# Kernel optimization log

Measured on AMD Instinct MI355X. Metric: run time of the kernel, lower is better.

The kernel has to match this reference:

```python
import jax, jax.numpy as jnp
import numpy as np

N_NODES = 50000
N_EDGES = 400000
NUM_GRAPHS = 64
D = 128
NUM_ACTIONS = 40


def setup_inputs() -> dict:
    key = jax.random.key(0)
    ks = jax.random.split(key, 20)
    s = 1.0 / np.sqrt(D)
    inp = {
        'inputs': jax.random.normal(ks[0], (N_NODES, D), jnp.float32),
        'src': jax.random.randint(ks[1], (N_EDGES,), 0, N_NODES, jnp.int32),
        'dst': jax.random.randint(ks[2], (N_EDGES,), 0, N_NODES, jnp.int32),
        'graph_ids': jnp.sort(jax.random.randint(ks[3], (N_NODES,), 0, NUM_GRAPHS, jnp.int32)),
        'init_feats': jax.random.normal(ks[4], (N_NODES, D), jnp.float32),
        'init_graph_ids': jnp.sort(jax.random.randint(ks[5], (N_NODES,), 0, NUM_GRAPHS, jnp.int32)),
        'lead_feats': jax.random.normal(ks[6], (N_NODES, D), jnp.float32),
        'lead_graph_ids': jnp.sort(jax.random.randint(ks[7], (N_NODES,), 0, NUM_GRAPHS, jnp.int32)),
        'W1': jax.random.normal(ks[8], (D, D), jnp.float32) * s,
        'b1': jnp.zeros((D,), jnp.float32),
        'W2': jax.random.normal(ks[9], (D, D), jnp.float32) * s,
        'b2': jnp.zeros((D,), jnp.float32),
        'W3': jax.random.normal(ks[10], (D, D), jnp.float32) * s,
        'b3': jnp.zeros((D,), jnp.float32),
        'fc1_W': jax.random.normal(ks[11], (D, D), jnp.float32) * s,
        'fc1_b': jnp.zeros((D,), jnp.float32),
        'fc2_W': jax.random.normal(ks[12], (D, NUM_ACTIONS), jnp.float32) * s,
        'fc2_b': jnp.zeros((NUM_ACTIONS,), jnp.float32),
    }
    return inp


def _pool(feats, gids):
    # SumPooling over a batched graph -> [B, D]
    return jax.ops.segment_sum(feats, gids, num_segments=NUM_GRAPHS)


def _ggin_layer(h, src, dst, graph_ids, ctx_per_graph, W, b):
    # neighbor sum aggregation (message passing over edge list)
    agg = jax.ops.segment_sum(h[src], dst, num_segments=N_NODES)  # [N, D]
    h_global = _pool(h, graph_ids)                                # [B, D]
    ctx = (h_global + ctx_per_graph)[graph_ids]                   # broadcast per-graph context to nodes
    return (h + agg + ctx) @ W + b


def reference(inputs, src, dst, graph_ids, init_feats, init_graph_ids,
              lead_feats, lead_graph_ids, W1, b1, W2, b2, W3, b3,
              fc1_W, fc1_b, fc2_W, fc2_b):
    h_initial = _pool(init_feats, init_graph_ids)   # [B, D]
    h_lead = _pool(lead_feats, lead_graph_ids)      # [B, D]
    ctx = h_initial + h_lead

    h = jax.nn.relu(_ggin_layer(inputs, src, dst, graph_ids, ctx, W1, b1))
    h = jax.nn.relu(_ggin_layer(h, src, dst, graph_ids, ctx, W2, b2))
    h = jax.nn.relu(_ggin_layer(h, src, dst, graph_ids, ctx, W3, b3))

    h_global = _pool(h, graph_ids)                  # [B, D]
    h_fc = jax.nn.relu(h_global @ fc1_W + fc1_b)
    return h_fc @ fc2_W + fc2_b                     # [B, num_actions]
```

## Files before the change

kernel.cpp:

```cpp
#include <hip/hip_runtime.h>

#define D 128
#define NGRAPH 64
#define NACT 40
#define SCAN_TPB 256
#define SCAN_EPT 8
#define SCAN_CHUNK 2048
#define GNODES 8
#define POOL_CHUNK 64

typedef __attribute__((ext_vector_type(8))) short bf16x8;
typedef __attribute__((ext_vector_type(4))) float f32x4;
typedef __attribute__((ext_vector_type(8))) unsigned short us8;

__device__ inline unsigned short f2b(float f) {
    unsigned u = __float_as_uint(f);
    return (unsigned short)((u + 0x7FFFu + ((u >> 16) & 1u)) >> 16);
}
__device__ inline float b2f(unsigned short h) {
    return __uint_as_float(((unsigned)h) << 16);
}

__global__ void pool3_kernel(const float* __restrict__ f0, const int* __restrict__ g0, float* o0,
                             const float* __restrict__ f1, const int* __restrict__ g1, float* o1,
                             const float* __restrict__ f2, const int* __restrict__ g2, float* o2,
                             int n_nodes) {
    const float* feats; const int* gids; float* out;
    if (blockIdx.y == 0)      { feats = f0; gids = g0; out = o0; }
    else if (blockIdx.y == 1) { feats = f1; gids = g1; out = o1; }
    else                      { feats = f2; gids = g2; out = o2; }
    int t = threadIdx.x;
    int start = blockIdx.x * POOL_CHUNK;
    int end = start + POOL_CHUNK;
    if (end > n_nodes) end = n_nodes;
    if (start >= end) return;
    int cur = gids[start];
    float acc = 0.f;
    int r = start;
    while (r < end) {
        if (r + 3 < end && gids[r] == cur && gids[r + 3] == cur) {
            float v0 = feats[(size_t)r * D + t];
            float v1 = feats[(size_t)(r + 1) * D + t];
            float v2 = feats[(size_t)(r + 2) * D + t];
            float v3 = feats[(size_t)(r + 3) * D + t];
            acc += (v0 + v1) + (v2 + v3);
            r += 4;
            continue;
        }
        int g = gids[r];
        if (g != cur) { atomicAdd(&out[cur * D + t], acc); acc = 0.f; cur = g; }
        acc += feats[(size_t)r * D + t];
        ++r;
    }
    atomicAdd(&out[cur * D + t], acc);
}

__global__ void pool_b16_kernel(const unsigned short* __restrict__ feats,
                                const int* __restrict__ gids, float* __restrict__ out,
                                int n_nodes) {
    int t = threadIdx.x;
    int start = blockIdx.x * POOL_CHUNK;
    int end = start + POOL_CHUNK;
    if (end > n_nodes) end = n_nodes;
    if (start >= end) return;
    int cur = gids[start];
    float acc = 0.f;
    int r = start;
    while (r < end) {
        if (r + 3 < end && gids[r] == cur && gids[r + 3] == cur) {
            float v0 = b2f(feats[(size_t)r * D + t]);
            float v1 = b2f(feats[(size_t)(r + 1) * D + t]);
            float v2 = b2f(feats[(size_t)(r + 2) * D + t]);
            float v3 = b2f(feats[(size_t)(r + 3) * D + t]);
            acc += (v0 + v1) + (v2 + v3);
            r += 4;
            continue;
        }
        int g = gids[r];
        if (g != cur) { atomicAdd(&out[cur * D + t], acc); acc = 0.f; cur = g; }
        acc += b2f(feats[(size_t)r * D + t]);
        ++r;
    }
    atomicAdd(&out[cur * D + t], acc);
}

__global__ void ctxw_kernel(const float* __restrict__ hg, const float* __restrict__ ctx,
                            const float* __restrict__ W, const float* __restrict__ b,
                            float* __restrict__ out) {
    __shared__ float row[D];
    int g = blockIdx.x, t = threadIdx.x;
    row[t] = hg[g * D + t] + ctx[g * D + t];
    __syncthreads();
    float acc = b[t];
#pragma unroll 4
    for (int k = 0; k < D; ++k) acc = fmaf(row[k], W[k * D + t], acc);
    out[g * D + t] = acc;
}

__global__ void conv_kernel(const float4* __restrict__ in4, ushort4* __restrict__ out4, int n4) {
    int stride = gridDim.x * blockDim.x;
    for (int i = blockIdx.x * blockDim.x + threadIdx.x; i < n4; i += stride) {
        float4 v = in4[i];
        ushort4 o;
        o.x = f2b(v.x); o.y = f2b(v.y); o.z = f2b(v.z); o.w = f2b(v.w);
        out4[i] = o;
    }
}

__global__ void wconv_kernel(const float* __restrict__ W0, const float* __restrict__ W1,
                             const float* __restrict__ W2, unsigned short* __restrict__ WTb) {
    const float* W = blockIdx.y == 0 ? W0 : (blockIdx.y == 1 ? W1 : W2);
    unsigned short* WT = WTb + blockIdx.y * (D * D);
    int idx = blockIdx.x * 256 + threadIdx.x;
    int n = idx >> 7, k = idx & 127;
    WT[n * D + k] = f2b(W[k * D + n]);
}

__global__ __launch_bounds__(256) void mm_mfma(const unsigned short* __restrict__ Hb,
                                               const unsigned short* __restrict__ WT,
                                               unsigned short* __restrict__ X, int n_rows) {
    __shared__ unsigned short aT[64 * 136];
    __shared__ unsigned short bT[128 * 136];
    int t = threadIdx.x;
    int r0 = blockIdx.x * 64;

    for (int i = t; i < 1024; i += 256) {
        int r = i >> 4, kq = i & 15;
        us8 v = {0, 0, 0, 0, 0, 0, 0, 0};
        if (r0 + r < n_rows) v = *(const us8*)(Hb + (size_t)(r0 + r) * D + kq * 8);
        *(us8*)&aT[r * 136 + kq * 8] = v;
    }
    for (int i = t; i < 2048; i += 256) {
        int n = i >> 4, kq = i & 15;
        *(us8*)&bT[n * 136 + kq * 8] = *(const us8*)(WT + n * D + kq * 8);
    }
    __syncthreads();

    int lane = t & 63;
    int rbase = (t >> 6) * 16;
    int arow = lane & 15, kgrp = lane >> 4;
    f32x4 acc[8];
#pragma unroll
    for (int i = 0; i < 8; ++i) acc[i] = (f32x4){0.f, 0.f, 0.f, 0.f};

#pragma unroll
    for (int kc = 0; kc < 4; ++kc) {
        bf16x8 a = *(bf16x8*)&aT[(rbase + arow) * 136 + kc * 32 + kgrp * 8];
#pragma unroll
        for (int nt = 0; nt < 8; ++nt) {
            bf16x8 b = *(bf16x8*)&bT[(nt * 16 + arow) * 136 + kc * 32 + kgrp * 8];
            acc[nt] = __builtin_amdgcn_mfma_f32_16x16x32_bf16(a, b, acc[nt], 0, 0, 0);
        }
    }

    int rr = rbase + kgrp * 4;
#pragma unroll
    for (int nt = 0; nt < 8; ++nt) {
#pragma unroll
        for (int j = 0; j < 4; ++j) {
            int r = r0 + rr + j;
            if (r < n_rows) X[(size_t)r * D + nt * 16 + arow] = f2b(acc[nt][j]);
        }
    }
}

__global__ void hist_kernel(const int* __restrict__ dst, int* __restrict__ counts, int n_edges) {
    int stride = gridDim.x * blockDim.x;
    for (int e = blockIdx.x * blockDim.x + threadIdx.x; e < n_edges; e += stride)
        atomicAdd(&counts[dst[e]], 1);
}

__global__ void scanA_kernel(const int* __restrict__ counts, int* __restrict__ rowptr,
                             int* __restrict__ blocksums, int n) {
    __shared__ int smem[SCAN_TPB];
    int b = blockIdx.x, t = threadIdx.x;
    int i0 = b * SCAN_CHUNK + t * SCAN_EPT;
    int e[SCAN_EPT];
#pragma unroll
    for (int j = 0; j < SCAN_EPT; ++j) {
        int i = i0 + j;
        e[j] = (i < n) ? counts[i] : 0;
    }
#pragma unroll
    for (int j = 1; j < SCAN_EPT; ++j) e[j] += e[j - 1];
    smem[t] = e[SCAN_EPT - 1];
    __syncthreads();
    for (int off = 1; off < SCAN_TPB; off <<= 1) {
        int u = (t >= off) ? smem[t - off] : 0;
        __syncthreads();
        smem[t] += u;
        __syncthreads();
    }
    int excl = t ? smem[t - 1] : 0;
#pragma unroll
    for (int j = 0; j < SCAN_EPT; ++j) {
        int i = i0 + j;
        if (i < n) rowptr[i + 1] = excl + e[j];
    }
    if (t == SCAN_TPB - 1) blocksums[b] = smem[t];
    if (b == 0 && t == 0) rowptr[0] = 0;
}

__global__ void scanC_kernel(int* __restrict__ rowptr, int* __restrict__ cursor,
                             const int* __restrict__ blocksums, int n) {
    __shared__ int off_s;
    int b = blockIdx.x, t = threadIdx.x;
    if (t == 0) {
        int a = 0;
        for (int i = 0; i < b; ++i) a += blocksums[i];
        off_s = a;
    }
    __syncthreads();
    int off = off_s;
    int i0 = b * SCAN_CHUNK + t * SCAN_EPT;
#pragma unroll
    for (int j = 0; j < SCAN_EPT; ++j) {
        int i = i0 + j;
        if (i < n) {
            int v = rowptr[i + 1] + off;
            rowptr[i + 1] = v;
            if (i + 1 < n) cursor[i + 1] = v;
        }
    }
    if (b == 0 && t == 0) cursor[0] = 0;
}

__global__ void fill_kernel(const int* __restrict__ src, const int* __restrict__ dst,
                            int* __restrict__ cursor, int* __restrict__ srcs, int n_edges) {
    int stride = gridDim.x * blockDim.x;
    for (int e = blockIdx.x * blockDim.x + threadIdx.x; e < n_edges; e += stride) {
        int pos = atomicAdd(&cursor[dst[e]], 1);
        srcs[pos] = src[e];
    }
}

__global__ __launch_bounds__(256) void gather_kernel(const unsigned short* __restrict__ Xb,
        const int* __restrict__ rowptr, const int* __restrict__ srcs,
        const int* __restrict__ gids, const float4* __restrict__ ctxgW4,
        unsigned short* __restrict__ Hb, int n_nodes) {
    int n = blockIdx.x * GNODES + (threadIdx.x >> 5);
    if (n >= n_nodes) return;
    int q = threadIdx.x & 31;
    int beg = rowptr[n], end = rowptr[n + 1];
    ushort4 a = *(const ushort4*)(Xb + (size_t)n * D + q * 4);
    float4 c = ctxgW4[(size_t)gids[n] * 32 + q];
    float ax = b2f(a.x) + c.x, ay = b2f(a.y) + c.y;
    float az = b2f(a.z) + c.z, aw = b2f(a.w) + c.w;
    int e = beg;
    for (; e + 4 <= end; e += 4) {
        int s0 = srcs[e], s1 = srcs[e + 1], s2 = srcs[e + 2], s3 = srcs[e + 3];
        ushort4 v0 = *(const ushort4*)(Xb + (size_t)s0 * D + q * 4);
        ushort4 v1 = *(const ushort4*)(Xb + (size_t)s1 * D + q * 4);
        ushort4 v2 = *(const ushort4*)(Xb + (size_t)s2 * D + q * 4);
        ushort4 v3 = *(const ushort4*)(Xb + (size_t)s3 * D + q * 4);
        ax += (b2f(v0.x) + b2f(v1.x)) + (b2f(v2.x) + b2f(v3.x));
        ay += (b2f(v0.y) + b2f(v1.y)) + (b2f(v2.y) + b2f(v3.y));
        az += (b2f(v0.z) + b2f(v1.z)) + (b2f(v2.z) + b2f(v3.z));
        aw += (b2f(v0.w) + b2f(v1.w)) + (b2f(v2.w) + b2f(v3.w));
    }
    for (; e < end; ++e) {
        ushort4 v = *(const ushort4*)(Xb + (size_t)srcs[e] * D + q * 4);
        ax += b2f(v.x); ay += b2f(v.y); az += b2f(v.z); aw += b2f(v.w);
    }
    ushort4 o;
    o.x = f2b(fmaxf(ax, 0.f)); o.y = f2b(fmaxf(ay, 0.f));
    o.z = f2b(fmaxf(az, 0.f)); o.w = f2b(fmaxf(aw, 0.f));
    *(ushort4*)(Hb + (size_t)n * D + q * 4) = o;
}

__global__ void head_kernel(const float* __restrict__ hg,
                            const float* __restrict__ fc1W, const float* __restrict__ fc1b,
                            const float* __restrict__ fc2W, const float* __restrict__ fc2b,
                            float* __restrict__ out) {
    __shared__ float row[D];
    __shared__ float hfc[D];
    int g = blockIdx.x, t = threadIdx.x;
    row[t] = hg[g * D + t];
    __syncthreads();
    float acc = fc1b[t];
#pragma unroll 4
    for (int k = 0; k < D; ++k) acc = fmaf(row[k], fc1W[k * D + t], acc);
    hfc[t] = fmaxf(acc, 0.f);
    __syncthreads();
    if (t < NACT) {
        float o = fc2b[t];
#pragma unroll 4
        for (int k = 0; k < D; ++k) o = fmaf(hfc[k], fc2W[k * NACT + t], o);
        out[g * NACT + t] = o;
    }
}

extern "C" void kernel_launch(void* const* d_in, const int* in_sizes, int n_in,
                              void* d_out, int out_size, void* d_ws, size_t ws_size,
                              hipStream_t stream) {
    const float* inputs     = (const float*)d_in[0];
    const int*   src        = (const int*)d_in[1];
    const int*   dst        = (const int*)d_in[2];
    const int*   graph_ids  = (const int*)d_in[3];
    const float* init_feats = (const float*)d_in[4];
    const int*   init_gids  = (const int*)d_in[5];
    const float* lead_feats = (const float*)d_in[6];
    const int*   lead_gids  = (const int*)d_in[7];
    const float* Wmat[3] = { (const float*)d_in[8], (const float*)d_in[10], (const float*)d_in[12] };
    const float* bvec[3] = { (const float*)d_in[9], (const float*)d_in[11], (const float*)d_in[13] };
    const float* fc1W = (const float*)d_in[14];
    const float* fc1b = (const float*)d_in[15];
    const float* fc2W = (const float*)d_in[16];
    const float* fc2b = (const float*)d_in[17];
    float* out = (float*)d_out;

    const int n_nodes = in_sizes[0] / D;
    const int n_edges = in_sizes[1];

    unsigned char* p = (unsigned char*)d_ws;
    float* ctx    = (float*)p;                          p += NGRAPH * D * sizeof(float);
    float* hg     = (float*)p;                          p += 4 * NGRAPH * D * sizeof(float);
    int*   counts = (int*)p;                            p += (size_t)n_nodes * sizeof(int);
    size_t zero_bytes = (size_t)(p - (unsigned char*)d_ws);
    int*   rowptr = (int*)p;                            p += ((size_t)n_nodes + 1) * sizeof(int);
    int*   blocksums = (int*)p;                         p += 64 * sizeof(int);
    float* ctxgW  = (float*)p;                          p += NGRAPH * D * sizeof(float);
    int*   srcs   = (int*)p;                            p += (size_t)n_edges * sizeof(int);
    p = (unsigned char*)(((uintptr_t)p + 15) & ~(uintptr_t)15);
    unsigned short* Hbf = (unsigned short*)p;           p += (size_t)n_nodes * D * sizeof(short);
    unsigned short* Xbf = (unsigned short*)p;           p += (size_t)n_nodes * D * sizeof(short);
    unsigned short* WTb = (unsigned short*)p;           p += 3 * D * D * sizeof(short);

    const int pool_blocks = (n_nodes + POOL_CHUNK - 1) / POOL_CHUNK;
    const int mm_blocks = (n_nodes + 63) / 64;
    const int scan_blocks = (n_nodes + SCAN_CHUNK - 1) / SCAN_CHUNK;
    const int gather_blocks = (n_nodes + GNODES - 1) / GNODES;
    const int n4 = n_nodes * D / 4;

    hipMemsetAsync(ctx, 0, zero_bytes, stream);

    hist_kernel<<<1024, 256, 0, stream>>>(dst, counts, n_edges);
    scanA_kernel<<<scan_blocks, SCAN_TPB, 0, stream>>>(counts, rowptr, blocksums, n_nodes);
    scanC_kernel<<<scan_blocks, SCAN_TPB, 0, stream>>>(rowptr, counts, blocksums, n_nodes);
    fill_kernel<<<1024, 256, 0, stream>>>(src, dst, counts, srcs, n_edges);

    conv_kernel<<<2048, 256, 0, stream>>>((const float4*)inputs, (ushort4*)Hbf, n4);
    wconv_kernel<<<dim3(64, 3), 256, 0, stream>>>(Wmat[0], Wmat[1], Wmat[2], WTb);

    pool3_kernel<<<dim3(pool_blocks, 3), D, 0, stream>>>(
        init_feats, init_gids, ctx, lead_feats, lead_gids, ctx,
        inputs, graph_ids, hg, n_nodes);

    for (int layer = 0; layer < 3; ++layer) {
        float* hgL = hg + layer * NGRAPH * D;
        ctxw_kernel<<<NGRAPH, D, 0, stream>>>(hgL, ctx, Wmat[layer], bvec[layer], ctxgW);
        mm_mfma<<<mm_blocks, 256, 0, stream>>>(Hbf, WTb + layer * D * D, Xbf, n_nodes);
        gather_kernel<<<gather_blocks, 256, 0, stream>>>(Xbf, rowptr, srcs, graph_ids,
                                                         (const float4*)ctxgW, Hbf, n_nodes);
        pool_b16_kernel<<<pool_blocks, D, 0, stream>>>(Hbf, graph_ids,
                                                       hg + (layer + 1) * NGRAPH * D, n_nodes);
    }

    head_kernel<<<NGRAPH, D, 0, stream>>>(hg + 3 * NGRAPH * D, fc1W, fc1b, fc2W, fc2b, out);
}
```

Before: 416.0 us.

## Fuse pooling into gather, ctx matvec into matmul, and bf16 conversion into pooling

Global sum pooling of each layer's output moves into the gather kernel. Each 8-node block reduces its nodes per graph in shared memory and issues atomics, which removes the separate pass that re-read the bf16 hidden states. The per-graph context matvec runs as extra blocks of the MFMA matmul launch, and the fp32-to-bf16 conversion of the inputs is folded into the initial pooling kernel. This cuts kernel launches and memory passes. The trade-off is many more global atomics on the 64×128 pooled array, one set per 8-node block instead of per 64-node chunk.

```diff
diff --git a/kernel.cpp b/kernel.cpp
--- a/kernel.cpp
+++ b/kernel.cpp
@@ -24,11 +24,11 @@
 __global__ void pool3_kernel(const float* __restrict__ f0, const int* __restrict__ g0, float* o0,
                              const float* __restrict__ f1, const int* __restrict__ g1, float* o1,
                              const float* __restrict__ f2, const int* __restrict__ g2, float* o2,
-                             int n_nodes) {
-    const float* feats; const int* gids; float* out;
+                             unsigned short* __restrict__ Hbf, int n_nodes) {
+    const float* feats; const int* gids; float* out; bool conv = false;
     if (blockIdx.y == 0)      { feats = f0; gids = g0; out = o0; }
     else if (blockIdx.y == 1) { feats = f1; gids = g1; out = o1; }
-    else                      { feats = f2; gids = g2; out = o2; }
+    else                      { feats = f2; gids = g2; out = o2; conv = true; }
     int t = threadIdx.x;
     int start = blockIdx.x * POOL_CHUNK;
     int end = start + POOL_CHUNK;
@@ -43,87 +43,52 @@
             float v1 = feats[(size_t)(r + 1) * D + t];
             float v2 = feats[(size_t)(r + 2) * D + t];
             float v3 = feats[(size_t)(r + 3) * D + t];
+            if (conv) {
+                Hbf[(size_t)r * D + t]       = f2b(v0);
+                Hbf[(size_t)(r + 1) * D + t] = f2b(v1);
+                Hbf[(size_t)(r + 2) * D + t] = f2b(v2);
+                Hbf[(size_t)(r + 3) * D + t] = f2b(v3);
+            }
             acc += (v0 + v1) + (v2 + v3);
             r += 4;
             continue;
         }
         int g = gids[r];
         if (g != cur) { atomicAdd(&out[cur * D + t], acc); acc = 0.f; cur = g; }
-        acc += feats[(size_t)r * D + t];
+        float v = feats[(size_t)r * D + t];
+        if (conv) Hbf[(size_t)r * D + t] = f2b(v);
+        acc += v;
         ++r;
     }
     atomicAdd(&out[cur * D + t], acc);
 }
 
-__global__ void pool_b16_kernel(const unsigned short* __restrict__ feats,
-                                const int* __restrict__ gids, float* __restrict__ out,
-                                int n_nodes) {
-    int t = threadIdx.x;
-    int start = blockIdx.x * POOL_CHUNK;
-    int end = start + POOL_CHUNK;
-    if (end > n_nodes) end = n_nodes;
-    if (start >= end) return;
-    int cur = gids[start];
-    float acc = 0.f;
-    int r = start;
-    while (r < end) {
-        if (r + 3 < end && gids[r] == cur && gids[r + 3] == cur) {
-            float v0 = b2f(feats[(size_t)r * D + t]);
-            float v1 = b2f(feats[(size_t)(r + 1) * D + t]);
-            float v2 = b2f(feats[(size_t)(r + 2) * D + t]);
-            float v3 = b2f(feats[(size_t)(r + 3) * D + t]);
-            acc += (v0 + v1) + (v2 + v3);
-            r += 4;
-            continue;
-        }
-        int g = gids[r];
-        if (g != cur) { atomicAdd(&out[cur * D + t], acc); acc = 0.f; cur = g; }
-        acc += b2f(feats[(size_t)r * D + t]);
-        ++r;
-    }
-    atomicAdd(&out[cur * D + t], acc);
-}
-
-__global__ void ctxw_kernel(const float* __restrict__ hg, const float* __restrict__ ctx,
-                            const float* __restrict__ W, const float* __restrict__ b,
-                            float* __restrict__ out) {
-    __shared__ float row[D];
-    int g = blockIdx.x, t = threadIdx.x;
-    row[t] = hg[g * D + t] + ctx[g * D + t];
-    __syncthreads();
-    float acc = b[t];
-#pragma unroll 4
-    for (int k = 0; k < D; ++k) acc = fmaf(row[k], W[k * D + t], acc);
-    out[g * D + t] = acc;
-}
-
-__global__ void conv_kernel(const float4* __restrict__ in4, ushort4* __restrict__ out4, int n4) {
-    int stride = gridDim.x * blockDim.x;
-    for (int i = blockIdx.x * blockDim.x + threadIdx.x; i < n4; i += stride) {
-        float4 v = in4[i];
-        ushort4 o;
-        o.x = f2b(v.x); o.y = f2b(v.y); o.z = f2b(v.z); o.w = f2b(v.w);
-        out4[i] = o;
-    }
-}
-
-__global__ void wconv_kernel(const float* __restrict__ W0, const float* __restrict__ W1,
-                             const float* __restrict__ W2, unsigned short* __restrict__ WTb) {
-    const float* W = blockIdx.y == 0 ? W0 : (blockIdx.y == 1 ? W1 : W2);
-    unsigned short* WT = WTb + blockIdx.y * (D * D);
-    int idx = blockIdx.x * 256 + threadIdx.x;
-    int n = idx >> 7, k = idx & 127;
-    WT[n * D + k] = f2b(W[k * D + n]);
-}
-
-__global__ __launch_bounds__(256) void mm_mfma(const unsigned short* __restrict__ Hb,
-                                               const unsigned short* __restrict__ WT,
-                                               unsigned short* __restrict__ X, int n_rows) {
+__global__ __launch_bounds__(256) void mm_ctxw_kernel(
+        const unsigned short* __restrict__ Hb, const unsigned short* __restrict__ WT,
+        unsigned short* __restrict__ X,
+        const float* __restrict__ hg, const float* __restrict__ ctx,
+        const float* __restrict__ Wf, const float* __restrict__ bias,
+        float* __restrict__ ctxgW, int n_rows, int mm_blocks) {
     __shared__ unsigned short aT[64 * 136];
     __shared__ unsigned short bT[128 * 136];
+    __shared__ float row2[2][D];
     int t = threadIdx.x;
+
+    if ((int)blockIdx.x >= mm_blocks) {
+        int bb = blockIdx.x - mm_blocks;
+        int half = t >> 7;
+        int g = bb * 2 + half;
+        int tc = t & 127;
+        row2[half][tc] = hg[g * D + tc] + ctx[g * D + tc];
+        __syncthreads();
+        float acc = bias[tc];
+#pragma unroll 4
+        for (int k = 0; k < D; ++k) acc = fmaf(row2[half][k], Wf[k * D + tc], acc);
+        ctxgW[g * D + tc] = acc;
+        return;
+    }
+
     int r0 = blockIdx.x * 64;
-
     for (int i = t; i < 1024; i += 256) {
         int r = i >> 4, kq = i & 15;
         us8 v = {0, 0, 0, 0, 0, 0, 0, 0};
@@ -234,38 +199,78 @@
     }
 }
 
-__global__ __launch_bounds__(256) void gather_kernel(const unsigned short* __restrict__ Xb,
+__global__ __launch_bounds__(256) void gather_pool_kernel(
+        const unsigned short* __restrict__ Xb,
         const int* __restrict__ rowptr, const int* __restrict__ srcs,
         const int* __restrict__ gids, const float4* __restrict__ ctxgW4,
-        unsigned short* __restrict__ Hb, int n_nodes) {
-    int n = blockIdx.x * GNODES + (threadIdx.x >> 5);
-    if (n >= n_nodes) return;
+        unsigned short* __restrict__ Hb, float* __restrict__ hg_next, int n_nodes) {
+    __shared__ float pool_lds[GNODES][D];
+    __shared__ int g_lds[GNODES];
+    int w = threadIdx.x >> 5;
     int q = threadIdx.x & 31;
-    int beg = rowptr[n], end = rowptr[n + 1];
-    ushort4 a = *(const ushort4*)(Xb + (size_t)n * D + q * 4);
-    float4 c = ctxgW4[(size_t)gids[n] * 32 + q];
-    float ax = b2f(a.x) + c.x, ay = b2f(a.y) + c.y;
-    float az = b2f(a.z) + c.z, aw = b2f(a.w) + c.w;
-    int e = beg;
-    for (; e + 4 <= end; e += 4) {
-        int s0 = srcs[e], s1 = srcs[e + 1], s2 = srcs[e + 2], s3 = srcs[e + 3];
-        ushort4 v0 = *(const ushort4*)(Xb + (size_t)s0 * D + q * 4);
-        ushort4 v1 = *(const ushort4*)(Xb + (size_t)s1 * D + q * 4);
-        ushort4 v2 = *(const ushort4*)(Xb + (size_t)s2 * D + q * 4);
-        ushort4 v3 = *(const ushort4*)(Xb + (size_t)s3 * D + q * 4);
-        ax += (b2f(v0.x) + b2f(v1.x)) + (b2f(v2.x) + b2f(v3.x));
-        ay += (b2f(v0.y) + b2f(v1.y)) + (b2f(v2.y) + b2f(v3.y));
-        az += (b2f(v0.z) + b2f(v1.z)) + (b2f(v2.z) + b2f(v3.z));
-        aw += (b2f(v0.w) + b2f(v1.w)) + (b2f(v2.w) + b2f(v3.w));
-    }
-    for (; e < end; ++e) {
-        ushort4 v = *(const ushort4*)(Xb + (size_t)srcs[e] * D + q * 4);
-        ax += b2f(v.x); ay += b2f(v.y); az += b2f(v.z); aw += b2f(v.w);
-    }
-    ushort4 o;
-    o.x = f2b(fmaxf(ax, 0.f)); o.y = f2b(fmaxf(ay, 0.f));
-    o.z = f2b(fmaxf(az, 0.f)); o.w = f2b(fmaxf(aw, 0.f));
-    *(ushort4*)(Hb + (size_t)n * D + q * 4) = o;
+    int n = blockIdx.x * GNODES + w;
+    bool active = (n < n_nodes);
+    float ax = 0.f, ay = 0.f, az = 0.f, aw = 0.f;
+    int g = -1;
+    if (active) {
+        g = gids[n];
+        int beg = rowptr[n], end = rowptr[n + 1];
+        ushort4 a = *(const ushort4*)(Xb + (size_t)n * D + q * 4);
+        float4 c = ctxgW4[(size_t)g * 32 + q];
+        ax = b2f(a.x) + c.x; ay = b2f(a.y) + c.y;
+        az = b2f(a.z) + c.z; aw = b2f(a.w) + c.w;
+        int e = beg;
+        for (; e + 4 <= end; e += 4) {
+            int s0 = srcs[e], s1 = srcs[e + 1], s2 = srcs[e + 2], s3 = srcs[e + 3];
+            ushort4 v0 = *(const ushort4*)(Xb + (size_t)s0 * D + q * 4);
+            ushort4 v1 = *(const ushort4*)(Xb + (size_t)s1 * D + q * 4);
+            ushort4 v2 = *(const ushort4*)(Xb + (size_t)s2 * D + q * 4);
+            ushort4 v3 = *(const ushort4*)(Xb + (size_t)s3 * D + q * 4);
+            ax += (b2f(v0.x) + b2f(v1.x)) + (b2f(v2.x) + b2f(v3.x));
+            ay += (b2f(v0.y) + b2f(v1.y)) + (b2f(v2.y) + b2f(v3.y));
+            az += (b2f(v0.z) + b2f(v1.z)) + (b2f(v2.z) + b2f(v3.z));
+            aw += (b2f(v0.w) + b2f(v1.w)) + (b2f(v2.w) + b2f(v3.w));
+        }
+        for (; e < end; ++e) {
+            ushort4 v = *(const ushort4*)(Xb + (size_t)srcs[e] * D + q * 4);
+            ax += b2f(v.x); ay += b2f(v.y); az += b2f(v.z); aw += b2f(v.w);
+        }
+        ax = fmaxf(ax, 0.f); ay = fmaxf(ay, 0.f);
+        az = fmaxf(az, 0.f); aw = fmaxf(aw, 0.f);
+        ushort4 o;
+        o.x = f2b(ax); o.y = f2b(ay); o.z = f2b(az); o.w = f2b(aw);
+        *(ushort4*)(Hb + (size_t)n * D + q * 4) = o;
+    }
+    if (q == 0) g_lds[w] = g;
+    pool_lds[w][q * 4 + 0] = ax;
+    pool_lds[w][q * 4 + 1] = ay;
+    pool_lds[w][q * 4 + 2] = az;
+    pool_lds[w][q * 4 + 3] = aw;
+    __syncthreads();
+    int gw = g_lds[w];
+    bool leader = (gw >= 0) && (w == 0 || g_lds[w - 1] != gw);
+    if (leader) {
+        float s0 = 0.f, s1 = 0.f, s2 = 0.f, s3 = 0.f;
+        for (int w2 = w; w2 < GNODES && g_lds[w2] == gw; ++w2) {
+            s0 += pool_lds[w2][q * 4 + 0];
+            s1 += pool_lds[w2][q * 4 + 1];
+            s2 += pool_lds[w2][q * 4 + 2];
+            s3 += pool_lds[w2][q * 4 + 3];
+        }
+        atomicAdd(&hg_next[gw * D + q * 4 + 0], s0);
+        atomicAdd(&hg_next[gw * D + q * 4 + 1], s1);
+        atomicAdd(&hg_next[gw * D + q * 4 + 2], s2);
+        atomicAdd(&hg_next[gw * D + q * 4 + 3], s3);
+    }
+}
+
+__global__ void wconv_kernel(const float* __restrict__ W0, const float* __restrict__ W1,
+                             const float* __restrict__ W2, unsigned short* __restrict__ WTb) {
+    const float* W = blockIdx.y == 0 ? W0 : (blockIdx.y == 1 ? W1 : W2);
+    unsigned short* WT = WTb + blockIdx.y * (D * D);
+    int idx = blockIdx.x * 256 + threadIdx.x;
+    int n = idx >> 7, k = idx & 127;
+    WT[n * D + k] = f2b(W[k * D + n]);
 }
 
 __global__ void head_kernel(const float* __restrict__ hg,
@@ -330,7 +335,6 @@
     const int mm_blocks = (n_nodes + 63) / 64;
     const int scan_blocks = (n_nodes + SCAN_CHUNK - 1) / SCAN_CHUNK;
     const int gather_blocks = (n_nodes + GNODES - 1) / GNODES;
-    const int n4 = n_nodes * D / 4;
 
     hipMemsetAsync(ctx, 0, zero_bytes, stream);
 
@@ -339,21 +343,20 @@
     scanC_kernel<<<scan_blocks, SCAN_TPB, 0, stream>>>(rowptr, counts, blocksums, n_nodes);
     fill_kernel<<<1024, 256, 0, stream>>>(src, dst, counts, srcs, n_edges);
 
-    conv_kernel<<<2048, 256, 0, stream>>>((const float4*)inputs, (ushort4*)Hbf, n4);
     wconv_kernel<<<dim3(64, 3), 256, 0, stream>>>(Wmat[0], Wmat[1], Wmat[2], WTb);
 
     pool3_kernel<<<dim3(pool_blocks, 3), D, 0, stream>>>(
         init_feats, init_gids, ctx, lead_feats, lead_gids, ctx,
-        inputs, graph_ids, hg, n_nodes);
+        inputs, graph_ids, hg, Hbf, n_nodes);
 
     for (int layer = 0; layer < 3; ++layer) {
         float* hgL = hg + layer * NGRAPH * D;
-        ctxw_kernel<<<NGRAPH, D, 0, stream>>>(hgL, ctx, Wmat[layer], bvec[layer], ctxgW);
-        mm_mfma<<<mm_blocks, 256, 0, stream>>>(Hbf, WTb + layer * D * D, Xbf, n_nodes);
-        gather_kernel<<<gather_blocks, 256, 0, stream>>>(Xbf, rowptr, srcs, graph_ids,
-                                                         (const float4*)ctxgW, Hbf, n_nodes);
-        pool_b16_kernel<<<pool_blocks, D, 0, stream>>>(Hbf, graph_ids,
-                                                       hg + (layer + 1) * NGRAPH * D, n_nodes);
+        mm_ctxw_kernel<<<mm_blocks + NGRAPH / 2, 256, 0, stream>>>(
+            Hbf, WTb + layer * D * D, Xbf,
+            hgL, ctx, Wmat[layer], bvec[layer], ctxgW, n_nodes, mm_blocks);
+        gather_pool_kernel<<<gather_blocks, 256, 0, stream>>>(
+            Xbf, rowptr, srcs, graph_ids, (const float4*)ctxgW,
+            Hbf, hg + (layer + 1) * NGRAPH * D, n_nodes);
     }
 
     head_kernel<<<NGRAPH, D, 0, stream>>>(hg + 3 * NGRAPH * D, fc1W, fc1b, fc2W, fc2b, out);
```

Result: slower. 469.5 us (+12.9%).
